# Kernel tuning notes

Hardware: AMD Instinct MI355X
Metric: run time of the kernel (lower is better)

The kernel has to match this reference:

```python
import jax, jax.numpy as jnp
import numpy as np

# Loss config: losses = [Supervised(weight=1), TemporalConsistency(padding=0.05, weight=1)]
PADDING_FRAC = 0.05
W_SUPERVISED = 1.0
W_TEMPORAL = 1.0


def setup_inputs() -> dict:
    key = jax.random.key(0)
    k1, k2 = jax.random.split(key)
    B, T, C, H, W = 4, 24, 4, 240, 320
    frames = jax.random.uniform(k1, (B, T, C, H, W), dtype=jnp.float32)
    # sparsify GT alpha so the (gt_alpha > 0) mask is non-trivial (fast-moving object occupies part of the frame)
    alpha = frames[:, :, 3:]
    frames = frames.at[:, :, 3:].set(jnp.where(alpha > 0.5, alpha, 0.0))
    renders = jax.random.uniform(k2, (B, T, C, H, W), dtype=jnp.float32)
    return {"frames": frames, "renders": renders}


def _l1(a, b, w, dims):
    # masked mean-abs-error over image dims, then mean over time axis 1 -> [B]
    err = jnp.sum(jnp.abs(a - b) * w, axis=dims)
    wsum = jnp.sum(w, axis=dims)
    wsum = wsum + (wsum == 0)  # avoid div by zero, matches torch weights + (weights==0)
    return (err / wsum).mean(axis=1)


def _supervised(frames, renders):
    gt_rgb, rend_rgb = frames[:, :, :3], renders[:, :, :3]
    gt_a, rend_a = frames[:, :, -1:], renders[:, :, -1:]
    mask = (gt_a > 0).astype(frames.dtype)
    dims = (2, 3, 4)
    alpha_in = _l1(gt_a, rend_a, mask, dims)
    alpha_out = _l1(gt_a, rend_a, 1.0 - mask, dims)
    rgb = _l1(gt_rgb * gt_a, rend_rgb * rend_a, mask, dims)
    return (alpha_in + alpha_out + rgb) / 3


def _normalize(t, dims):
    mean = t.mean(axis=dims, keepdims=True)
    std = t.std(axis=dims, keepdims=True)  # ddof=0 == torch unbiased=False
    std = std + (std == 0)
    return (t - mean) / std


def _zncc(a, b, pad):
    # a, b: [B, T, C, H, W]; per-(b,t) zero-normalized cross-correlation over (dy, dx) shifts
    B, T, C, H, W = a.shape
    dims = (2, 3, 4)
    a = _normalize(a, dims)
    b = _normalize(b, dims)
    BT = B * T
    lhs = a.reshape(1, BT, C, H, W)     # N=1, channels=BT, spatial=(C,H,W)
    rhs = b.reshape(BT, 1, C, H, W)     # one full-size kernel per group
    cc = jax.lax.conv_general_dilated(
        lhs, rhs,
        window_strides=(1, 1, 1),
        padding=[(0, 0), (pad, pad), (pad, pad)],
        dimension_numbers=("NCDHW", "OIDHW", "NCDHW"),
        feature_group_count=BT,
    )  # [1, BT, 1, 2p+1, 2p+1]; jax conv is cross-correlation like torch
    cc = cc / (C * H * W)
    return cc.reshape(B, T, cc.shape[-2], cc.shape[-1])


def _temporal_consistency(renders):
    pad = int(PADDING_FRAC * renders.shape[-1])
    z = _zncc(renders[:, :-1], renders[:, 1:], pad)  # [B, T-1, 2p+1, 2p+1]
    return (1.0 - z.max(axis=(2, 3)).mean(axis=1)) / 2


def reference(frames, renders):
    sup = _supervised(frames, renders) * W_SUPERVISED
    tc = _temporal_consistency(renders) * W_TEMPORAL
    return jnp.stack([sup, tc], axis=1)  # [B, n_losses=2]
```

## Files before the change

### kernel.cpp

```cpp
#include <hip/hip_runtime.h>
#include <hip/hip_bf16.h>

#define B_    4
#define T_    24
#define C_    4
#define H_    240
#define W_    320
#define HW_   (H_*W_)
#define CHW_  (C_*HW_)
#define NF_   (B_*T_)
#define NPAIR_ (B_*(T_-1))
#define PAD_  16
#define ND_   33
#define HC_   16
#define NCH_  15

constexpr int PART_OFF = 0;
constexpr int MEAN_OFF = PART_OFF + NF_*8*6;
constexpr int ISTD_OFF = MEAN_OFF + NF_;
constexpr int Z_OFF    = ISTD_OFF + NF_;

typedef __attribute__((ext_vector_type(8))) __bf16 bf16x8;
typedef __attribute__((ext_vector_type(4))) float  f32x4;

static __device__ __forceinline__ unsigned short f2bf(float f) {
  unsigned u = __builtin_bit_cast(unsigned, f);
  unsigned r = (u + 0x7FFFu + ((u >> 16) & 1u)) >> 16;
  return (unsigned short)r;
}
static __device__ __forceinline__ unsigned pk2(float lo, float hi) {
  return (unsigned)f2bf(lo) | ((unsigned)f2bf(hi) << 16);
}

__global__ __launch_bounds__(256) void sup_stats_kernel(
    const float* __restrict__ frames, const float* __restrict__ renders,
    float* __restrict__ ws) {
  const int f = blockIdx.x >> 3;
  const int s = blockIdx.x & 7;
  const float* Fb = frames  + (size_t)f * CHW_;
  const float* Rb = renders + (size_t)f * CHW_;
  const int p0 = s * (HW_ / 8);
  const int p1 = p0 + HW_ / 8;
  float S1 = 0.f, S2 = 0.f, S3 = 0.f, MS = 0.f, SR = 0.f, SQ = 0.f;
  for (int p = p0 + (int)threadIdx.x; p < p1; p += 256) {
    float fa = Fb[3 * HW_ + p];
    float ra = Rb[3 * HW_ + p];
    float f0 = Fb[p], f1 = Fb[HW_ + p], f2 = Fb[2 * HW_ + p];
    float r0 = Rb[p], r1 = Rb[HW_ + p], r2 = Rb[2 * HW_ + p];
    float m = (fa > 0.f) ? 1.f : 0.f;
    float d = fabsf(fa - ra);
    S1 = fmaf(d, m, S1);
    S2 = fmaf(d, 1.f - m, S2);
    MS += m;
    float e = fabsf(f0 * fa - r0 * ra) + fabsf(f1 * fa - r1 * ra) +
              fabsf(f2 * fa - r2 * ra);
    S3 = fmaf(e, m, S3);
    SR += r0 + r1 + r2 + ra;
    SQ += r0 * r0 + r1 * r1 + r2 * r2 + ra * ra;
  }
  __shared__ float sm[4];
  float vals[6] = {S1, S2, S3, MS, SR, SQ};
  float* dst = ws + PART_OFF + (size_t)(f * 8 + s) * 6;
  const int wv = threadIdx.x >> 6, ln = threadIdx.x & 63;
  for (int k = 0; k < 6; ++k) {
    float v = vals[k];
    #pragma unroll
    for (int o = 32; o >= 1; o >>= 1) v += __shfl_down(v, o);
    __syncthreads();
    if (ln == 0) sm[wv] = v;
    __syncthreads();
    if (threadIdx.x == 0) dst[k] = sm[0] + sm[1] + sm[2] + sm[3];
  }
}

__global__ __launch_bounds__(128) void finalize_stats_kernel(
    float* __restrict__ ws, float* __restrict__ out) {
  __shared__ float term_s[NF_];
  const int f = threadIdx.x;
  if (f < NF_) {
    float S1 = 0, S2 = 0, S3 = 0, MS = 0, SR = 0, SQ = 0;
    for (int s = 0; s < 8; ++s) {
      const float* p = ws + PART_OFF + (size_t)(f * 8 + s) * 6;
      S1 += p[0]; S2 += p[1]; S3 += p[2]; MS += p[3]; SR += p[4]; SQ += p[5];
    }
    float mean = SR * (1.f / (float)CHW_);
    float var  = SQ * (1.f / (float)CHW_) - mean * mean;
    float sd   = sqrtf(fmaxf(var, 0.f));
    if (sd == 0.f) sd = 1.f;
    ws[MEAN_OFF + f] = mean;
    ws[ISTD_OFF + f] = 1.f / sd;
    float w1 = MS;               if (w1 == 0.f) w1 = 1.f;
    float w2 = (float)HW_ - MS;  if (w2 == 0.f) w2 = 1.f;
    term_s[f] = (S1 / w1 + S2 / w2 + S3 / w1) * (1.f / 3.f);
  }
  __syncthreads();
  if (threadIdx.x < B_) {
    float acc = 0.f;
    for (int t = 0; t < T_; ++t) acc += term_s[threadIdx.x * T_ + t];
    out[2 * threadIdx.x] = acc * (1.f / (float)T_);
  }
}

__global__ __launch_bounds__(256, 2) void zncc_mfma_kernel(
    const float* __restrict__ renders, float* __restrict__ ws) {
  const int pair  = blockIdx.x / NCH_;
  const int chunk = blockIdx.x - pair * NCH_;
  const int h0 = chunk * HC_;
  const int bb = pair / (T_ - 1);
  const int tt = pair - bb * (T_ - 1);
  const int fa = bb * T_ + tt;
  const int fb = fa + 1;
  const float ma = ws[MEAN_OFF + fa], ia = ws[ISTD_OFF + fa];
  const float mb = ws[MEAN_OFF + fb], ib = ws[ISTD_OFF + fb];
  const int tid = threadIdx.x;
  const int wv = tid >> 6, ln = tid & 63;
  const int g = ln >> 4, r = ln & 15;

  __shared__ bf16x8   a_s8[64 * 41];
  __shared__ unsigned bs_[HC_][368];

  f32x4 acc[3][3];
  #pragma unroll
  for (int mi = 0; mi < 3; ++mi)
    #pragma unroll
    for (int ni = 0; ni < 3; ++ni)
      acc[mi][ni] = (f32x4){0.f, 0.f, 0.f, 0.f};

  for (int c = 0; c < C_; ++c) {
    __syncthreads();
    {
      const float* Ag = renders + ((size_t)fa * C_ + c) * HW_;
      unsigned short* a_su = (unsigned short*)a_s8;
      for (int q = tid; q < 64 * 80; q += 256) {
        const int si = q / 80;
        const int c4 = (q - si * 80) << 2;
        const int gr = h0 - 16 + si;
        ushort4 s;
        if (gr >= 0 && gr < H_) {
          float4 v = *(const float4*)(Ag + (size_t)gr * W_ + c4);
          s.x = f2bf((v.x - ma) * ia);
          s.y = f2bf((v.y - ma) * ia);
          s.z = f2bf((v.z - ma) * ia);
          s.w = f2bf((v.w - ma) * ia);
        } else {
          s.x = 0; s.y = 0; s.z = 0; s.w = 0;
        }
        *(ushort4*)(a_su + si * 328 + c4) = s;
      }
    }
    {
      const float* Bg = renders + ((size_t)fb * C_ + c) * HW_;
      for (int xq = tid; xq < HC_ * 92; xq += 256) {
        const int hr = xq / 92;
        const int x0 = (xq - hr * 92) << 2;
        const float* brow = Bg + (size_t)(h0 + hr) * W_;
        float wv5[5];
        const int wbase = x0 - 32;
        #pragma unroll
        for (int k = 0; k < 5; ++k) {
          const int ww = wbase + k;
          wv5[k] = (ww >= 0 && ww < W_) ? (brow[ww] - mb) * ib : 0.f;
        }
        uint4 pk;
        pk.x = pk2(wv5[0], wv5[1]);
        pk.y = pk2(wv5[1], wv5[2]);
        pk.z = pk2(wv5[2], wv5[3]);
        pk.w = pk2(wv5[3], wv5[4]);
        *(uint4*)&bs_[hr][x0] = pk;
      }
    }
    __syncthreads();
    for (int ho = 0; ho < HC_ / 4; ++ho) {
      const int hh = ho * 4 + wv;
      const unsigned* bsrow = bs_[hh];
      for (int kw = 0; kw < 10; ++kw) {
        bf16x8 af[3];
        #pragma unroll
        for (int mi = 0; mi < 3; ++mi)
          af[mi] = a_s8[(hh + 16 * mi + r) * 41 + 4 * kw + g];
        bf16x8 bfr[3];
        #pragma unroll
        for (int ni = 0; ni < 3; ++ni) {
          const int pe = 32 * kw + 8 * g + 48 - 16 * ni - r;
          union { unsigned u[4]; bf16x8 v; } bu;
          bu.u[0] = bsrow[pe];
          bu.u[1] = bsrow[pe + 2];
          bu.u[2] = bsrow[pe + 4];
          bu.u[3] = bsrow[pe + 6];
          bfr[ni] = bu.v;
        }
        #pragma unroll
        for (int mi = 0; mi < 3; ++mi)
          #pragma unroll
          for (int ni = 0; ni < 3; ++ni)
            acc[mi][ni] = __builtin_amdgcn_mfma_f32_16x16x32_bf16(
                af[mi], bfr[ni], acc[mi][ni], 0, 0, 0);
      }
    }
  }

  float* z = ws + Z_OFF + (size_t)pair * (ND_ * ND_);
  #pragma unroll
  for (int mi = 0; mi < 3; ++mi) {
    #pragma unroll
    for (int i = 0; i < 4; ++i) {
      const int m = 16 * mi + 4 * g + i;
      if (m < ND_) {
        #pragma unroll
        for (int ni = 0; ni < 3; ++ni) {
          const int n = 16 * ni + r;
          if (n < ND_)
            atomicAdd(&z[m * ND_ + n], acc[mi][ni][i] * (1.f / (float)CHW_));
        }
      }
    }
  }
}

__global__ __launch_bounds__(256) void tc_kernel(
    const float* __restrict__ ws, float* __restrict__ out) {
  const int b = blockIdx.x;
  __shared__ float sm[4];
  const int wv = threadIdx.x >> 6, ln = threadIdx.x & 63;
  float summax = 0.f;
  for (int t = 0; t < T_ - 1; ++t) {
    const float* z = ws + Z_OFF + (size_t)(b * (T_ - 1) + t) * (ND_ * ND_);
    float m = -3.4e38f;
    for (int i = threadIdx.x; i < ND_ * ND_; i += 256) m = fmaxf(m, z[i]);
    #pragma unroll
    for (int o = 32; o >= 1; o >>= 1) m = fmaxf(m, __shfl_down(m, o));
    __syncthreads();
    if (ln == 0) sm[wv] = m;
    __syncthreads();
    if (threadIdx.x == 0)
      summax += fmaxf(fmaxf(sm[0], sm[1]), fmaxf(sm[2], sm[3]));
  }
  if (threadIdx.x == 0)
    out[2 * b + 1] = (1.f - summax * (1.f / (float)(T_ - 1))) * 0.5f;
}

extern "C" void kernel_launch(void* const* d_in, const int* in_sizes, int n_in,
                              void* d_out, int out_size, void* d_ws, size_t ws_size,
                              hipStream_t stream) {
  const float* frames  = (const float*)d_in[0];
  const float* renders = (const float*)d_in[1];
  float* out = (float*)d_out;
  float* ws  = (float*)d_ws;
  hipLaunchKernelGGL(sup_stats_kernel, dim3(NF_ * 8), dim3(256), 0, stream,
                     frames, renders, ws);
  hipLaunchKernelGGL(finalize_stats_kernel, dim3(1), dim3(128), 0, stream, ws, out);
  hipMemsetAsync((char*)d_ws + (size_t)Z_OFF * 4, 0,
                 (size_t)NPAIR_ * ND_ * ND_ * 4, stream);
  hipLaunchKernelGGL(zncc_mfma_kernel, dim3(NPAIR_ * NCH_), dim3(256), 0, stream,
                     renders, ws);
  hipLaunchKernelGGL(tc_kernel, dim3(B_), dim3(256), 0, stream, ws, out);
}
```

Baseline: 532.3 us.

## Widen ZNCC blocks to 512 threads, vectorize loads, parallelize max reduction

```diff
diff --git a/kernel.cpp b/kernel.cpp
--- a/kernel.cpp
+++ b/kernel.cpp
@@ -19,9 +19,11 @@
 constexpr int MEAN_OFF = PART_OFF + NF_*8*6;
 constexpr int ISTD_OFF = MEAN_OFF + NF_;
 constexpr int Z_OFF    = ISTD_OFF + NF_;
+constexpr int ZMAX_OFF = Z_OFF + NPAIR_*ND_*ND_;
 
 typedef __attribute__((ext_vector_type(8))) __bf16 bf16x8;
 typedef __attribute__((ext_vector_type(4))) float  f32x4;
+typedef __attribute__((ext_vector_type(8))) unsigned short ushort8;
 
 static __device__ __forceinline__ unsigned short f2bf(float f) {
   unsigned u = __builtin_bit_cast(unsigned, f);
@@ -40,23 +42,39 @@
   const float* Fb = frames  + (size_t)f * CHW_;
   const float* Rb = renders + (size_t)f * CHW_;
   const int p0 = s * (HW_ / 8);
-  const int p1 = p0 + HW_ / 8;
   float S1 = 0.f, S2 = 0.f, S3 = 0.f, MS = 0.f, SR = 0.f, SQ = 0.f;
-  for (int p = p0 + (int)threadIdx.x; p < p1; p += 256) {
-    float fa = Fb[3 * HW_ + p];
-    float ra = Rb[3 * HW_ + p];
-    float f0 = Fb[p], f1 = Fb[HW_ + p], f2 = Fb[2 * HW_ + p];
-    float r0 = Rb[p], r1 = Rb[HW_ + p], r2 = Rb[2 * HW_ + p];
-    float m = (fa > 0.f) ? 1.f : 0.f;
-    float d = fabsf(fa - ra);
-    S1 = fmaf(d, m, S1);
-    S2 = fmaf(d, 1.f - m, S2);
-    MS += m;
-    float e = fabsf(f0 * fa - r0 * ra) + fabsf(f1 * fa - r1 * ra) +
-              fabsf(f2 * fa - r2 * ra);
-    S3 = fmaf(e, m, S3);
-    SR += r0 + r1 + r2 + ra;
-    SQ += r0 * r0 + r1 * r1 + r2 * r2 + ra * ra;
+  for (int q = (int)threadIdx.x; q < (HW_ / 8) / 4; q += 256) {
+    const int p = p0 + q * 4;
+    float4 f0 = *(const float4*)(Fb + p);
+    float4 f1 = *(const float4*)(Fb + HW_ + p);
+    float4 f2 = *(const float4*)(Fb + 2 * HW_ + p);
+    float4 fa = *(const float4*)(Fb + 3 * HW_ + p);
+    float4 r0 = *(const float4*)(Rb + p);
+    float4 r1 = *(const float4*)(Rb + HW_ + p);
+    float4 r2 = *(const float4*)(Rb + 2 * HW_ + p);
+    float4 ra = *(const float4*)(Rb + 3 * HW_ + p);
+    const float F0[4] = {f0.x, f0.y, f0.z, f0.w};
+    const float F1[4] = {f1.x, f1.y, f1.z, f1.w};
+    const float F2[4] = {f2.x, f2.y, f2.z, f2.w};
+    const float FA[4] = {fa.x, fa.y, fa.z, fa.w};
+    const float R0[4] = {r0.x, r0.y, r0.z, r0.w};
+    const float R1[4] = {r1.x, r1.y, r1.z, r1.w};
+    const float R2[4] = {r2.x, r2.y, r2.z, r2.w};
+    const float RA[4] = {ra.x, ra.y, ra.z, ra.w};
+    #pragma unroll
+    for (int k = 0; k < 4; ++k) {
+      float m = (FA[k] > 0.f) ? 1.f : 0.f;
+      float d = fabsf(FA[k] - RA[k]);
+      S1 = fmaf(d, m, S1);
+      S2 = fmaf(d, 1.f - m, S2);
+      MS += m;
+      float e = fabsf(F0[k] * FA[k] - R0[k] * RA[k]) +
+                fabsf(F1[k] * FA[k] - R1[k] * RA[k]) +
+                fabsf(F2[k] * FA[k] - R2[k] * RA[k]);
+      S3 = fmaf(e, m, S3);
+      SR += R0[k] + R1[k] + R2[k] + RA[k];
+      SQ += R0[k] * R0[k] + R1[k] * R1[k] + R2[k] * R2[k] + RA[k] * RA[k];
+    }
   }
   __shared__ float sm[4];
   float vals[6] = {S1, S2, S3, MS, SR, SQ};
@@ -101,7 +119,7 @@
   }
 }
 
-__global__ __launch_bounds__(256, 2) void zncc_mfma_kernel(
+__global__ __launch_bounds__(512, 4) void zncc_mfma_kernel(
     const float* __restrict__ renders, float* __restrict__ ws) {
   const int pair  = blockIdx.x / NCH_;
   const int chunk = blockIdx.x - pair * NCH_;
@@ -116,8 +134,8 @@
   const int wv = tid >> 6, ln = tid & 63;
   const int g = ln >> 4, r = ln & 15;
 
-  __shared__ bf16x8   a_s8[64 * 41];
-  __shared__ unsigned bs_[HC_][368];
+  __shared__ alignas(16) unsigned short a_su[64 * 328];
+  __shared__ alignas(16) unsigned bs_[HC_][368];
 
   f32x4 acc[3][3];
   #pragma unroll
@@ -130,27 +148,26 @@
     __syncthreads();
     {
       const float* Ag = renders + ((size_t)fa * C_ + c) * HW_;
-      unsigned short* a_su = (unsigned short*)a_s8;
-      for (int q = tid; q < 64 * 80; q += 256) {
-        const int si = q / 80;
-        const int c4 = (q - si * 80) << 2;
+      for (int q = tid; q < 64 * 40; q += 512) {
+        const int si = q / 40;
+        const int j8 = (q - si * 40) << 3;
         const int gr = h0 - 16 + si;
-        ushort4 s;
+        ushort8 sv = (ushort8)0;
         if (gr >= 0 && gr < H_) {
-          float4 v = *(const float4*)(Ag + (size_t)gr * W_ + c4);
-          s.x = f2bf((v.x - ma) * ia);
-          s.y = f2bf((v.y - ma) * ia);
-          s.z = f2bf((v.z - ma) * ia);
-          s.w = f2bf((v.w - ma) * ia);
-        } else {
-          s.x = 0; s.y = 0; s.z = 0; s.w = 0;
+          const float* src = Ag + (size_t)gr * W_ + j8;
+          float4 v0 = *(const float4*)(src);
+          float4 v1 = *(const float4*)(src + 4);
+          sv[0] = f2bf((v0.x - ma) * ia); sv[1] = f2bf((v0.y - ma) * ia);
+          sv[2] = f2bf((v0.z - ma) * ia); sv[3] = f2bf((v0.w - ma) * ia);
+          sv[4] = f2bf((v1.x - ma) * ia); sv[5] = f2bf((v1.y - ma) * ia);
+          sv[6] = f2bf((v1.z - ma) * ia); sv[7] = f2bf((v1.w - ma) * ia);
         }
-        *(ushort4*)(a_su + si * 328 + c4) = s;
+        *(ushort8*)(a_su + si * 328 + j8) = sv;
       }
     }
     {
       const float* Bg = renders + ((size_t)fb * C_ + c) * HW_;
-      for (int xq = tid; xq < HC_ * 92; xq += 256) {
+      for (int xq = tid; xq < HC_ * 92; xq += 512) {
         const int hr = xq / 92;
         const int x0 = (xq - hr * 92) << 2;
         const float* brow = Bg + (size_t)(h0 + hr) * W_;
@@ -170,14 +187,16 @@
       }
     }
     __syncthreads();
-    for (int ho = 0; ho < HC_ / 4; ++ho) {
-      const int hh = ho * 4 + wv;
-      const unsigned* bsrow = bs_[hh];
+    for (int ho = 0; ho < 2; ++ho) {
+      const int hh = ho * 8 + wv;
+      const unsigned* bsrow = &bs_[hh][0];
+      const unsigned short* arow = a_su + (hh + r) * 328 + g * 8;
+      #pragma unroll
       for (int kw = 0; kw < 10; ++kw) {
         bf16x8 af[3];
         #pragma unroll
         for (int mi = 0; mi < 3; ++mi)
-          af[mi] = a_s8[(hh + 16 * mi + r) * 41 + 4 * kw + g];
+          af[mi] = *(const bf16x8*)(arow + mi * (16 * 328) + kw * 32);
         bf16x8 bfr[3];
         #pragma unroll
         for (int ni = 0; ni < 3; ++ni) {
@@ -199,44 +218,67 @@
     }
   }
 
-  float* z = ws + Z_OFF + (size_t)pair * (ND_ * ND_);
-  #pragma unroll
-  for (int mi = 0; mi < 3; ++mi) {
-    #pragma unroll
-    for (int i = 0; i < 4; ++i) {
-      const int m = 16 * mi + 4 * g + i;
-      if (m < ND_) {
-        #pragma unroll
-        for (int ni = 0; ni < 3; ++ni) {
-          const int n = 16 * ni + r;
-          if (n < ND_)
-            atomicAdd(&z[m * ND_ + n], acc[mi][ni][i] * (1.f / (float)CHW_));
+  __syncthreads();
+  f32x4* red = (f32x4*)a_su;
+  if (wv >= 4) {
+    f32x4* dst = red + ((wv - 4) * 64 + ln) * 9;
+    #pragma unroll
+    for (int mi = 0; mi < 3; ++mi)
+      #pragma unroll
+      for (int ni = 0; ni < 3; ++ni)
+        dst[mi * 3 + ni] = acc[mi][ni];
+  }
+  __syncthreads();
+  if (wv < 4) {
+    const f32x4* src = red + (wv * 64 + ln) * 9;
+    #pragma unroll
+    for (int mi = 0; mi < 3; ++mi)
+      #pragma unroll
+      for (int ni = 0; ni < 3; ++ni)
+        acc[mi][ni] += src[mi * 3 + ni];
+    float* z = ws + Z_OFF + (size_t)pair * (ND_ * ND_);
+    #pragma unroll
+    for (int mi = 0; mi < 3; ++mi) {
+      #pragma unroll
+      for (int i = 0; i < 4; ++i) {
+        const int m = 16 * mi + 4 * g + i;
+        if (m < ND_) {
+          #pragma unroll
+          for (int ni = 0; ni < 3; ++ni) {
+            const int n = 16 * ni + r;
+            if (n < ND_)
+              atomicAdd(&z[m * ND_ + n], acc[mi][ni][i] * (1.f / (float)CHW_));
+          }
         }
       }
     }
   }
 }
 
-__global__ __launch_bounds__(256) void tc_kernel(
-    const float* __restrict__ ws, float* __restrict__ out) {
-  const int b = blockIdx.x;
+__global__ __launch_bounds__(256) void tc_max_kernel(
+    const float* __restrict__ ws, float* __restrict__ wso) {
+  const int pair = blockIdx.x;
+  const float* z = ws + Z_OFF + (size_t)pair * (ND_ * ND_);
+  float m = -3.4e38f;
+  for (int i = threadIdx.x; i < ND_ * ND_; i += 256) m = fmaxf(m, z[i]);
+  #pragma unroll
+  for (int o = 32; o >= 1; o >>= 1) m = fmaxf(m, __shfl_down(m, o));
   __shared__ float sm[4];
   const int wv = threadIdx.x >> 6, ln = threadIdx.x & 63;
-  float summax = 0.f;
-  for (int t = 0; t < T_ - 1; ++t) {
-    const float* z = ws + Z_OFF + (size_t)(b * (T_ - 1) + t) * (ND_ * ND_);
-    float m = -3.4e38f;
-    for (int i = threadIdx.x; i < ND_ * ND_; i += 256) m = fmaxf(m, z[i]);
-    #pragma unroll
-    for (int o = 32; o >= 1; o >>= 1) m = fmaxf(m, __shfl_down(m, o));
-    __syncthreads();
-    if (ln == 0) sm[wv] = m;
-    __syncthreads();
-    if (threadIdx.x == 0)
-      summax += fmaxf(fmaxf(sm[0], sm[1]), fmaxf(sm[2], sm[3]));
-  }
+  if (ln == 0) sm[wv] = m;
+  __syncthreads();
   if (threadIdx.x == 0)
-    out[2 * b + 1] = (1.f - summax * (1.f / (float)(T_ - 1))) * 0.5f;
+    wso[ZMAX_OFF + pair] = fmaxf(fmaxf(sm[0], sm[1]), fmaxf(sm[2], sm[3]));
+}
+
+__global__ __launch_bounds__(128) void tc_final_kernel(
+    const float* __restrict__ ws, float* __restrict__ out) {
+  if (threadIdx.x < B_) {
+    float s = 0.f;
+    for (int t = 0; t < T_ - 1; ++t)
+      s += ws[ZMAX_OFF + threadIdx.x * (T_ - 1) + t];
+    out[2 * threadIdx.x + 1] = (1.f - s * (1.f / (float)(T_ - 1))) * 0.5f;
+  }
 }
 
 extern "C" void kernel_launch(void* const* d_in, const int* in_sizes, int n_in,
@@ -251,7 +293,8 @@
   hipLaunchKernelGGL(finalize_stats_kernel, dim3(1), dim3(128), 0, stream, ws, out);
   hipMemsetAsync((char*)d_ws + (size_t)Z_OFF * 4, 0,
                  (size_t)NPAIR_ * ND_ * ND_ * 4, stream);
-  hipLaunchKernelGGL(zncc_mfma_kernel, dim3(NPAIR_ * NCH_), dim3(256), 0, stream,
+  hipLaunchKernelGGL(zncc_mfma_kernel, dim3(NPAIR_ * NCH_), dim3(512), 0, stream,
                      renders, ws);
-  hipLaunchKernelGGL(tc_kernel, dim3(B_), dim3(256), 0, stream, ws, out);
-}
+  hipLaunchKernelGGL(tc_max_kernel, dim3(NPAIR_), dim3(256), 0, stream, ws, ws);
+  hipLaunchKernelGGL(tc_final_kernel, dim3(1), dim3(128), 0, stream, ws, out);
+}
```

New measurement: 433.1 us. 1.23x faster.
